# Performance work log

Hardware: AMD Instinct MI355X
Metric: run time of the kernel (lower is better)

## Reference

```python
import jax, jax.numpy as jnp
import numpy as np

# ---- geometry constants (from init_kwargs options) ----
VIEWS, NDET, NX, NY = 360, 736, 512, 512
DVOX, DDET = 0.7, 1.2858
DSO, DOD = 595.0, 490.6
DSD = DSO + DOD
STEP = 0.0174533
END_ANGLE = STEP * VIEWS  # ~2*pi
EXTENT = 1


def _compute_indices():
    """CPU port of PixelIndexCal_cuda (fanflat mode, extent=1).
    Returns flat int64 indices of shape [NX*NY*VIEWS] (pixel-major, view inner)."""
    sVx, sVy = DVOX * NX, DVOX * NY
    alphas = np.linspace(0.0, END_ANGLE, VIEWS, endpoint=False)
    indX, indY = np.meshgrid(np.arange(NX, dtype=np.float64),
                             np.arange(NY, dtype=np.float64), indexing='ij')
    idx_all = np.empty((NX * NY, VIEWS), dtype=np.int64)
    for a in range(VIEWS):
        alpha = -alphas[a]
        c, s = np.cos(alpha), np.sin(alpha)
        P0x = -(sVx / 2 - DVOX / 2)
        P0y = sVy / 2 - DVOX / 2
        rot = lambda px, py: (px * c + py * s, -px * s + py * c)
        Px_, Py_ = rot(P0x, P0y)
        Pxx, Pxy = rot(P0x + DVOX, P0y)
        Pyx, Pyy = rot(P0x, P0y - DVOX)
        Py_, Pxy, Pyy = Py_ / DDET, Pxy / DDET, Pyy / DDET
        dXx, dXy = Pxx - Px_, Pxy - Py_
        dYx, dYy = Pyx - Px_, Pyy - Py_
        # per-pixel rotated coords
        Pix = Px_ + indX * dXx + indY * dYx
        Piy = Py_ + indX * dXy + indY * dYy
        # fanflat: source at (DSO, 0); ray hits detector plane at x = DSO-DSD
        vectX = Pix - DSO
        t = -DSD / vectX
        det = Piy * t + NDET / 2.0
        det = np.clip(det, 1.0, NDET - 2.0)
        idx_all[:, a] = (det + NDET * a).astype(np.int64).ravel()
    return idx_all.reshape(-1)


def _conv(x, w, b):
    y = jax.lax.conv_general_dilated(x, w, (1, 1), 'SAME',
                                     dimension_numbers=('NCHW', 'OIHW', 'NCHW'))
    return y + b[None, :, None, None]


def setup_inputs() -> dict:
    key = jax.random.key(0)
    ks = jax.random.split(key, 16)
    lin_std = 1.0 / np.sqrt(NDET)
    conv_std = 1.0 / np.sqrt(64 * 9)
    inp = {
        'x': jax.random.normal(ks[0], (1, 1, VIEWS, NDET), jnp.float32),
        'indices': jnp.asarray(_compute_indices()),
        'w1': jax.random.normal(ks[1], (NDET, NDET), jnp.float32) * lin_std,
        'b1': jnp.zeros((NDET,), jnp.float32),
        'w2': jax.random.normal(ks[2], (NDET, NDET), jnp.float32) * lin_std,
        'b2': jnp.zeros((NDET,), jnp.float32),
        'conv_in_w': jax.random.normal(ks[3], (64, 1, 3, 3), jnp.float32) * (1.0 / 3.0),
        'conv_in_b': jnp.zeros((64,), jnp.float32),
        'blk_w1': jax.random.normal(ks[4], (11, 64, 64, 3, 3), jnp.float32) * conv_std,
        'blk_b1': jnp.zeros((11, 64), jnp.float32),
        'blk_w2': jax.random.normal(ks[5], (11, 64, 64, 3, 3), jnp.float32) * conv_std,
        'blk_b2': jnp.zeros((11, 64), jnp.float32),
        'conv_out_w': jax.random.normal(ks[6], (1, 64, 3, 3), jnp.float32) * conv_std,
        'conv_out_b': jnp.zeros((1,), jnp.float32),
    }
    return inp


def reference(x, indices, w1, b1, w2, b2, conv_in_w, conv_in_b,
              blk_w1, blk_b1, blk_w2, blk_b2, conv_out_w, conv_out_b):
    # convf: two per-detector-row Linear+ReLU over last dim (nDetecU)
    h = jax.nn.relu(x @ w1.T + b1)
    h = jax.nn.relu(h @ w2.T + b2)
    # BackProjNet (learn=False): gather + sum over views, scale, flip
    sino = h.reshape(-1, 1, VIEWS * NDET)
    g = sino[:, :, indices]                         # [B,1,NX*NY*VIEWS]
    g = g.reshape(-1, 1, NX * NY, VIEWS * EXTENT)
    img = g.sum(axis=3) * ((END_ANGLE - 0.0) / (2 * VIEWS * EXTENT))
    img = img.reshape(-1, 1, NX, NY)
    img = jnp.flip(img, axis=(2, 3))
    # rCNN refinement: conv(1->64)+ReLU, 11 residual blocks, conv(64->1)
    y = jax.nn.relu(_conv(img, conv_in_w, conv_in_b))
    for i in range(11):
        z = _conv(y, blk_w1[i], blk_b1[i])
        z = jax.nn.relu(z)
        z = _conv(z, blk_w2[i], blk_b2[i])
        y = jax.nn.relu(y + z)
    out = _conv(y, conv_out_w, conv_out_b)
    return out
```

## Files before the change

kernel.cpp:

```cpp
#include <hip/hip_runtime.h>

#define VIEWS 360
#define NDET 736
#define NX 512
#define NY 512
#define NPIX (NX * NY)

typedef unsigned short u16;
typedef __attribute__((ext_vector_type(8))) short bf16x8;
typedef __attribute__((ext_vector_type(4))) float f32x4;

__device__ __forceinline__ u16 f2bf(float f) {
  unsigned u = __float_as_uint(f);
  return (u16)((u + 0x7fffu + ((u >> 16) & 1u)) >> 16);
}

__global__ __launch_bounds__(256) void linear_relu_kernel(
    const float* __restrict__ in, const float* __restrict__ w,
    const float* __restrict__ b, float* __restrict__ out) {
  __shared__ __align__(16) float xin[NDET];
  const int v = blockIdx.x;
  const float4* src4 = (const float4*)(in + v * NDET);
  float4* dst4 = (float4*)xin;
  for (int k = threadIdx.x; k < NDET / 4; k += 256) dst4[k] = src4[k];
  __syncthreads();

  for (int d = threadIdx.x; d < NDET; d += 256) {
    const float4* w4 = (const float4*)(w + d * NDET);
    float acc = 0.f;
#pragma unroll 8
    for (int k = 0; k < NDET / 4; ++k) {
      float4 xv = ((const float4*)xin)[k];
      float4 wv = w4[k];
      acc = fmaf(xv.x, wv.x, acc);
      acc = fmaf(xv.y, wv.y, acc);
      acc = fmaf(xv.z, wv.z, acc);
      acc = fmaf(xv.w, wv.w, acc);
    }
    out[v * NDET + d] = fmaxf(acc + b[d], 0.f);
  }
}

__global__ __launch_bounds__(256) void backproj_kernel(
    const float* __restrict__ sino, const int* __restrict__ idx,
    float* __restrict__ img) {
  __shared__ int lidx[256 * 77];
  const int t = threadIdx.x;
  const int p_base = blockIdx.x * 256;

  float a0 = 0.f, a1 = 0.f, a2 = 0.f, a3 = 0.f;

#pragma unroll 1
  for (int c = 0; c < 5; ++c) {
    if (c) __syncthreads();
#pragma unroll
    for (int k = 0; k < 18; ++k) {
      const int f = k * 256 + t;
      const int row = f / 18, col4 = f % 18;
      int4 v = *(const int4*)&idx[(size_t)(p_base + row) * VIEWS + c * 72 +
                                  col4 * 4];
      int* dst = &lidx[row * 77 + col4 * 4];
      dst[0] = v.x; dst[1] = v.y; dst[2] = v.z; dst[3] = v.w;
    }
    __syncthreads();
    const int* myrow = &lidx[t * 77];
#pragma unroll
    for (int j = 0; j < 72; j += 4) {
      a0 += sino[myrow[j + 0]];
      a1 += sino[myrow[j + 1]];
      a2 += sino[myrow[j + 2]];
      a3 += sino[myrow[j + 3]];
    }
  }

  const int p = p_base + t;
  const int ix = p >> 9, iy = p & 511;
  img[(NX - 1 - ix) * NY + (NY - 1 - iy)] =
      ((a0 + a1) + (a2 + a3)) * 0.00872665f;
}

__device__ __forceinline__ void load9(const float* __restrict__ base, int gx,
                                      int gy, float v[9]) {
  const bool xm = gx > 0, xp = gx < NX - 1, ym = gy > 0, yp = gy < NY - 1;
  const float* c = base + gy * NX + gx;
  v[0] = (ym && xm) ? c[-NX - 1] : 0.f;
  v[1] = (ym)       ? c[-NX]     : 0.f;
  v[2] = (ym && xp) ? c[-NX + 1] : 0.f;
  v[3] = (xm)       ? c[-1]      : 0.f;
  v[4] =               c[0];
  v[5] = (xp)       ? c[1]       : 0.f;
  v[6] = (yp && xm) ? c[NX - 1]  : 0.f;
  v[7] = (yp)       ? c[NX]      : 0.f;
  v[8] = (yp && xp) ? c[NX + 1]  : 0.f;
}

__device__ __forceinline__ float dot9(float a, const float v[9],
                                      const float* __restrict__ w) {
  a = fmaf(v[0], w[0], a);
  a = fmaf(v[1], w[1], a);
  a = fmaf(v[2], w[2], a);
  a = fmaf(v[3], w[3], a);
  a = fmaf(v[4], w[4], a);
  a = fmaf(v[5], w[5], a);
  a = fmaf(v[6], w[6], a);
  a = fmaf(v[7], w[7], a);
  a = fmaf(v[8], w[8], a);
  return a;
}

__global__ __launch_bounds__(256) void conv_in_kernel(
    const float* __restrict__ in, const float* __restrict__ w,
    const float* __restrict__ b, float* __restrict__ out) {
  const int p = blockIdx.x * 256 + threadIdx.x;
  const int gx = p & (NX - 1), gy = p >> 9;
  float v[9];
  load9(in, gx, gy, v);
  float4* o = (float4*)(out + (size_t)p * 64);
#pragma unroll
  for (int oq = 0; oq < 16; ++oq) {
    float4 r;
    r.x = fmaxf(dot9(b[oq * 4 + 0], v, w + (oq * 4 + 0) * 9), 0.f);
    r.y = fmaxf(dot9(b[oq * 4 + 1], v, w + (oq * 4 + 1) * 9), 0.f);
    r.z = fmaxf(dot9(b[oq * 4 + 2], v, w + (oq * 4 + 2) * 9), 0.f);
    r.w = fmaxf(dot9(b[oq * 4 + 3], v, w + (oq * 4 + 3) * 9), 0.f);
    o[oq] = r;
  }
}

__global__ __launch_bounds__(256) void prep_weights_kernel(
    const float* __restrict__ bw1, const float* __restrict__ bw2,
    u16* __restrict__ wR) {
  const int g = blockIdx.x * 256 + threadIdx.x;
  if (g >= 22 * 36864) return;
  const int li = g / 36864, r1 = g % 36864;
  const int s = r1 / 2048, r2 = r1 % 2048;
  const int lane = r2 / 32, r3 = r2 % 32;
  const int mf = r3 / 8, j = r3 % 8;
  const int kb = s / 9, tap = s % 9;
  const int kg = lane >> 4, n = lane & 15;
  const int oc = mf * 16 + n;
  const int ic = kb * 32 + kg * 8 + j;
  const float* src = (li < 11) ? bw1 + li * 36864 : bw2 + (li - 11) * 36864;
  wR[g] = f2bf(src[(oc * 64 + ic) * 9 + tap]);
}

template <int IN_BF, int OUT_BF, int RELU, int ADDRES>
__global__ __launch_bounds__(256, 4) void conv64_mfma(
    const void* __restrict__ in_, const u16* __restrict__ wA,
    const float* __restrict__ bias, const float* __restrict__ res,
    void* __restrict__ out_) {
  __shared__ __align__(16) u16 lds[6 * 66 * 32];
  const int xb = (blockIdx.x & 7) * 64;
  const int yb = (int)(blockIdx.x >> 3) * 4;
  const int tid = threadIdx.x;
  const int wv = tid >> 6;
  const int lane = tid & 63;
  const int n = lane & 15;
  const int kg = lane >> 4;

  f32x4 acc[4][4];
#pragma unroll
  for (int i = 0; i < 4; ++i)
#pragma unroll
    for (int j = 0; j < 4; ++j) acc[i][j] = (f32x4){0.f, 0.f, 0.f, 0.f};

#pragma unroll 1
  for (int kb = 0; kb < 2; ++kb) {
    if (kb) __syncthreads();
#pragma unroll
    for (int it = 0; it < 7; ++it) {
      const int g = it * 256 + tid;
      if (g < 1584) {
        const int icq = g & 3;
        const int xr = g >> 2;
        const int x66 = xr % 66;
        const int r = xr / 66;
        const int y = yb - 1 + r;
        const int x = xb - 1 + x66;
        uint4 d = {0u, 0u, 0u, 0u};
        if ((unsigned)y < 512u && (unsigned)x < 512u) {
          const size_t gi =
              ((size_t)((y << 9) + x)) * 64 + kb * 32 + icq * 8;
          if (IN_BF) {
            d = *(const uint4*)&((const u16*)in_)[gi];
          } else {
            const float* s = &((const float*)in_)[gi];
            float4 f0 = *(const float4*)s;
            float4 f1 = *(const float4*)(s + 4);
            d.x = (unsigned)f2bf(f0.x) | ((unsigned)f2bf(f0.y) << 16);
            d.y = (unsigned)f2bf(f0.z) | ((unsigned)f2bf(f0.w) << 16);
            d.z = (unsigned)f2bf(f1.x) | ((unsigned)f2bf(f1.y) << 16);
            d.w = (unsigned)f2bf(f1.z) | ((unsigned)f2bf(f1.w) << 16);
          }
        }
        const int slot = icq ^ ((x66 >> 1) & 3);
        *(uint4*)&lds[(xr * 4 + slot) * 8] = d;
      }
    }
    __syncthreads();

#pragma unroll 3
    for (int tap = 0; tap < 9; ++tap) {
      const int s = kb * 9 + tap;
      bf16x8 av[4];
#pragma unroll
      for (int mf = 0; mf < 4; ++mf)
        av[mf] = *(const bf16x8*)&wA[((size_t)s * 64 + lane) * 32 + mf * 8];

      const int r = wv + tap / 3;
      const int dxp1 = tap % 3;

      bf16x8 bfr[4];
#pragma unroll
      for (int nf = 0; nf < 4; ++nf) {
        const int xi = dxp1 + nf * 16 + n;
        const int slot = kg ^ ((xi >> 1) & 3);
        bfr[nf] = *(const bf16x8*)&lds[((r * 66 + xi) * 4 + slot) * 8];
      }
#pragma unroll
      for (int mf = 0; mf < 4; ++mf)
#pragma unroll
        for (int nf = 0; nf < 4; ++nf)
          acc[mf][nf] = __builtin_amdgcn_mfma_f32_16x16x32_bf16(
              av[mf], bfr[nf], acc[mf][nf], 0, 0, 0);
    }
  }

  const int y = yb + wv;
#pragma unroll
  for (int mf = 0; mf < 4; ++mf) {
    const float4 bv = *(const float4*)&bias[mf * 16 + kg * 4];
#pragma unroll
    for (int nf = 0; nf < 4; ++nf) {
      const int x = xb + nf * 16 + n;
      const size_t base = ((size_t)((y << 9) + x)) * 64 + mf * 16 + kg * 4;
      float v0 = acc[mf][nf][0] + bv.x;
      float v1 = acc[mf][nf][1] + bv.y;
      float v2 = acc[mf][nf][2] + bv.z;
      float v3 = acc[mf][nf][3] + bv.w;
      if (ADDRES) {
        float4 rr = *(const float4*)&res[base];
        v0 += rr.x; v1 += rr.y; v2 += rr.z; v3 += rr.w;
      }
      if (RELU) {
        v0 = fmaxf(v0, 0.f); v1 = fmaxf(v1, 0.f);
        v2 = fmaxf(v2, 0.f); v3 = fmaxf(v3, 0.f);
      }
      if (OUT_BF) {
        uint2 pk;
        pk.x = (unsigned)f2bf(v0) | ((unsigned)f2bf(v1) << 16);
        pk.y = (unsigned)f2bf(v2) | ((unsigned)f2bf(v3) << 16);
        *(uint2*)&((u16*)out_)[base] = pk;
      } else {
        *(float4*)&((float*)out_)[base] = (float4){v0, v1, v2, v3};
      }
    }
  }
}

__global__ __launch_bounds__(256) void conv_out_kernel(
    const float* __restrict__ in, const float* __restrict__ w,
    const float* __restrict__ b, float* __restrict__ out) {
  const int p = blockIdx.x * 256 + threadIdx.x;
  const int gx = p & (NX - 1), gy = p >> 9;
  float a = b[0];
#pragma unroll
  for (int ty = 0; ty < 3; ++ty) {
#pragma unroll
    for (int tx = 0; tx < 3; ++tx) {
      const int yy = gy + ty - 1, xx = gx + tx - 1;
      if ((unsigned)yy < 512u && (unsigned)xx < 512u) {
        const float4* q = (const float4*)(in + ((size_t)((yy << 9) + xx)) * 64);
        const int tap = ty * 3 + tx;
#pragma unroll
        for (int i = 0; i < 16; ++i) {
          float4 d = q[i];
          a = fmaf(d.x, w[(i * 4 + 0) * 9 + tap], a);
          a = fmaf(d.y, w[(i * 4 + 1) * 9 + tap], a);
          a = fmaf(d.z, w[(i * 4 + 2) * 9 + tap], a);
          a = fmaf(d.w, w[(i * 4 + 3) * 9 + tap], a);
        }
      }
    }
  }
  out[p] = a;
}

extern "C" void kernel_launch(void* const* d_in, const int* in_sizes, int n_in,
                              void* d_out, int out_size, void* d_ws,
                              size_t ws_size, hipStream_t stream) {
  const float* x      = (const float*)d_in[0];
  const int*   indices= (const int*)d_in[1];
  const float* w1     = (const float*)d_in[2];
  const float* b1     = (const float*)d_in[3];
  const float* w2     = (const float*)d_in[4];
  const float* b2     = (const float*)d_in[5];
  const float* cin_w  = (const float*)d_in[6];
  const float* cin_b  = (const float*)d_in[7];
  const float* bw1    = (const float*)d_in[8];
  const float* bb1    = (const float*)d_in[9];
  const float* bw2    = (const float*)d_in[10];
  const float* bb2    = (const float*)d_in[11];
  const float* cout_w = (const float*)d_in[12];
  const float* cout_b = (const float*)d_in[13];

  float* ws   = (float*)d_ws;
  float* h1   = ws;
  float* h2   = h1 + VIEWS * NDET;
  float* img  = h2 + VIEWS * NDET;
  float* yf   = img + NPIX;
  u16*  zb    = (u16*)(yf + 64 * NPIX);
  u16*  wAll  = zb + 64 * NPIX;

  prep_weights_kernel<<<(22 * 36864 + 255) / 256, 256, 0, stream>>>(bw1, bw2,
                                                                    wAll);
  linear_relu_kernel<<<VIEWS, 256, 0, stream>>>(x, w1, b1, h1);
  linear_relu_kernel<<<VIEWS, 256, 0, stream>>>(h1, w2, b2, h2);
  backproj_kernel<<<NPIX / 256, 256, 0, stream>>>(h2, indices, img);
  conv_in_kernel<<<NPIX / 256, 256, 0, stream>>>(img, cin_w, cin_b, yf);

  for (int i = 0; i < 11; ++i) {
    conv64_mfma<0, 1, 1, 0><<<1024, 256, 0, stream>>>(
        yf, wAll + i * 36864, bb1 + i * 64, nullptr, zb);
    conv64_mfma<1, 0, 1, 1><<<1024, 256, 0, stream>>>(
        zb, wAll + (11 + i) * 36864, bb2 + i * 64, yf, yf);
  }
  conv_out_kernel<<<NPIX / 256, 256, 0, stream>>>(yf, cout_w, cout_b,
                                                  (float*)d_out);
}
```

Measured before the change: 1.835 ms.

## Keep bf16 activation copy, use direct global-to-LDS loads, batch linear rows

The residual stream is now also stored as bf16, so the first conv of each block reads a bf16 input instead of converting fp32 on the fly. The conv tile load uses global_load_lds with a zero-padding buffer for out-of-bounds pixels, which removes the register staging and the branchy zero fill. The linear layers now process four views per block so each weight row is reused across four rows of input. This adds an extra bf16 write per block and more workspace, and it relies on the direct-to-LDS write order matching the swizzled layout.

```diff
diff --git a/kernel.cpp b/kernel.cpp
--- a/kernel.cpp
+++ b/kernel.cpp
@@ -14,30 +14,71 @@
   unsigned u = __float_as_uint(f);
   return (u16)((u + 0x7fffu + ((u >> 16) & 1u)) >> 16);
 }
-
-__global__ __launch_bounds__(256) void linear_relu_kernel(
+__device__ __forceinline__ float bf2f(u16 v) {
+  return __uint_as_float(((unsigned)v) << 16);
+}
+
+__device__ __forceinline__ void gload_lds16(const void* g, void* l) {
+  __builtin_amdgcn_global_load_lds(
+      (const __attribute__((address_space(1))) void*)g,
+      (__attribute__((address_space(3))) void*)l, 16, 0, 0);
+}
+
+__global__ __launch_bounds__(256) void linear_relu4_kernel(
     const float* __restrict__ in, const float* __restrict__ w,
     const float* __restrict__ b, float* __restrict__ out) {
-  __shared__ __align__(16) float xin[NDET];
-  const int v = blockIdx.x;
-  const float4* src4 = (const float4*)(in + v * NDET);
-  float4* dst4 = (float4*)xin;
-  for (int k = threadIdx.x; k < NDET / 4; k += 256) dst4[k] = src4[k];
+  __shared__ __align__(16) float xin[4][NDET];
+  const int v0 = blockIdx.x * 4;
+  const int t = threadIdx.x;
+  for (int k = t; k < 4 * (NDET / 4); k += 256) {
+    const int row = k / (NDET / 4), c4 = k % (NDET / 4);
+    ((float4*)xin[row])[c4] = ((const float4*)(in + (size_t)(v0 + row) * NDET))[c4];
+  }
   __syncthreads();
 
-  for (int d = threadIdx.x; d < NDET; d += 256) {
-    const float4* w4 = (const float4*)(w + d * NDET);
-    float acc = 0.f;
-#pragma unroll 8
-    for (int k = 0; k < NDET / 4; ++k) {
-      float4 xv = ((const float4*)xin)[k];
-      float4 wv = w4[k];
-      acc = fmaf(xv.x, wv.x, acc);
-      acc = fmaf(xv.y, wv.y, acc);
-      acc = fmaf(xv.z, wv.z, acc);
-      acc = fmaf(xv.w, wv.w, acc);
-    }
-    out[v * NDET + d] = fmaxf(acc + b[d], 0.f);
+  const bool has2 = (t < NDET - 512);
+  const float4* w0 = (const float4*)(w + (size_t)t * NDET);
+  const float4* w1 = (const float4*)(w + (size_t)(t + 256) * NDET);
+  const float4* w2 = (const float4*)(w + (size_t)(has2 ? t + 512 : t) * NDET);
+
+  float acc[3][4];
+#pragma unroll
+  for (int j = 0; j < 3; ++j)
+#pragma unroll
+    for (int v = 0; v < 4; ++v) acc[j][v] = 0.f;
+
+#pragma unroll 2
+  for (int k = 0; k < NDET / 4; ++k) {
+    float4 xv0 = ((const float4*)xin[0])[k];
+    float4 xv1 = ((const float4*)xin[1])[k];
+    float4 xv2 = ((const float4*)xin[2])[k];
+    float4 xv3 = ((const float4*)xin[3])[k];
+    float4 wv;
+    wv = w0[k];
+    acc[0][0] = fmaf(xv0.x, wv.x, fmaf(xv0.y, wv.y, fmaf(xv0.z, wv.z, fmaf(xv0.w, wv.w, acc[0][0]))));
+    acc[0][1] = fmaf(xv1.x, wv.x, fmaf(xv1.y, wv.y, fmaf(xv1.z, wv.z, fmaf(xv1.w, wv.w, acc[0][1]))));
+    acc[0][2] = fmaf(xv2.x, wv.x, fmaf(xv2.y, wv.y, fmaf(xv2.z, wv.z, fmaf(xv2.w, wv.w, acc[0][2]))));
+    acc[0][3] = fmaf(xv3.x, wv.x, fmaf(xv3.y, wv.y, fmaf(xv3.z, wv.z, fmaf(xv3.w, wv.w, acc[0][3]))));
+    wv = w1[k];
+    acc[1][0] = fmaf(xv0.x, wv.x, fmaf(xv0.y, wv.y, fmaf(xv0.z, wv.z, fmaf(xv0.w, wv.w, acc[1][0]))));
+    acc[1][1] = fmaf(xv1.x, wv.x, fmaf(xv1.y, wv.y, fmaf(xv1.z, wv.z, fmaf(xv1.w, wv.w, acc[1][1]))));
+    acc[1][2] = fmaf(xv2.x, wv.x, fmaf(xv2.y, wv.y, fmaf(xv2.z, wv.z, fmaf(xv2.w, wv.w, acc[1][2]))));
+    acc[1][3] = fmaf(xv3.x, wv.x, fmaf(xv3.y, wv.y, fmaf(xv3.z, wv.z, fmaf(xv3.w, wv.w, acc[1][3]))));
+    wv = w2[k];
+    acc[2][0] = fmaf(xv0.x, wv.x, fmaf(xv0.y, wv.y, fmaf(xv0.z, wv.z, fmaf(xv0.w, wv.w, acc[2][0]))));
+    acc[2][1] = fmaf(xv1.x, wv.x, fmaf(xv1.y, wv.y, fmaf(xv1.z, wv.z, fmaf(xv1.w, wv.w, acc[2][1]))));
+    acc[2][2] = fmaf(xv2.x, wv.x, fmaf(xv2.y, wv.y, fmaf(xv2.z, wv.z, fmaf(xv2.w, wv.w, acc[2][2]))));
+    acc[2][3] = fmaf(xv3.x, wv.x, fmaf(xv3.y, wv.y, fmaf(xv3.z, wv.z, fmaf(xv3.w, wv.w, acc[2][3]))));
+  }
+
+  const float b0 = b[t], b1 = b[t + 256];
+  const float b2v = has2 ? b[t + 512] : 0.f;
+#pragma unroll
+  for (int v = 0; v < 4; ++v) {
+    float* o = out + (size_t)(v0 + v) * NDET;
+    o[t] = fmaxf(acc[0][v] + b0, 0.f);
+    o[t + 256] = fmaxf(acc[1][v] + b1, 0.f);
+    if (has2) o[t + 512] = fmaxf(acc[2][v] + b2v, 0.f);
   }
 }
 
@@ -110,20 +151,28 @@
 
 __global__ __launch_bounds__(256) void conv_in_kernel(
     const float* __restrict__ in, const float* __restrict__ w,
-    const float* __restrict__ b, float* __restrict__ out) {
+    const float* __restrict__ b, float* __restrict__ outf,
+    u16* __restrict__ outb) {
   const int p = blockIdx.x * 256 + threadIdx.x;
   const int gx = p & (NX - 1), gy = p >> 9;
   float v[9];
   load9(in, gx, gy, v);
-  float4* o = (float4*)(out + (size_t)p * 64);
-#pragma unroll
-  for (int oq = 0; oq < 16; ++oq) {
-    float4 r;
-    r.x = fmaxf(dot9(b[oq * 4 + 0], v, w + (oq * 4 + 0) * 9), 0.f);
-    r.y = fmaxf(dot9(b[oq * 4 + 1], v, w + (oq * 4 + 1) * 9), 0.f);
-    r.z = fmaxf(dot9(b[oq * 4 + 2], v, w + (oq * 4 + 2) * 9), 0.f);
-    r.w = fmaxf(dot9(b[oq * 4 + 3], v, w + (oq * 4 + 3) * 9), 0.f);
-    o[oq] = r;
+  float4* of = (float4*)(outf + (size_t)p * 64);
+  uint4* ob = (uint4*)(outb + (size_t)p * 64);
+#pragma unroll
+  for (int oq = 0; oq < 8; ++oq) {
+    float f[8];
+#pragma unroll
+    for (int c = 0; c < 8; ++c)
+      f[c] = fmaxf(dot9(b[oq * 8 + c], v, w + (oq * 8 + c) * 9), 0.f);
+    of[oq * 2 + 0] = (float4){f[0], f[1], f[2], f[3]};
+    of[oq * 2 + 1] = (float4){f[4], f[5], f[6], f[7]};
+    uint4 pk;
+    pk.x = (unsigned)f2bf(f[0]) | ((unsigned)f2bf(f[1]) << 16);
+    pk.y = (unsigned)f2bf(f[2]) | ((unsigned)f2bf(f[3]) << 16);
+    pk.z = (unsigned)f2bf(f[4]) | ((unsigned)f2bf(f[5]) << 16);
+    pk.w = (unsigned)f2bf(f[6]) | ((unsigned)f2bf(f[7]) << 16);
+    ob[oq] = pk;
   }
 }
 
@@ -132,6 +181,7 @@
     u16* __restrict__ wR) {
   const int g = blockIdx.x * 256 + threadIdx.x;
   if (g >= 22 * 36864) return;
+  if (g < 32) wR[22 * 36864 + g] = 0;
   const int li = g / 36864, r1 = g % 36864;
   const int s = r1 / 2048, r2 = r1 % 2048;
   const int lane = r2 / 32, r3 = r2 % 32;
@@ -144,11 +194,12 @@
   wR[g] = f2bf(src[(oc * 64 + ic) * 9 + tap]);
 }
 
-template <int IN_BF, int OUT_BF, int RELU, int ADDRES>
+template <int ADDRES, int DUALOUT>
 __global__ __launch_bounds__(256, 4) void conv64_mfma(
-    const void* __restrict__ in_, const u16* __restrict__ wA,
+    const u16* __restrict__ in_, const u16* __restrict__ wA,
     const float* __restrict__ bias, const float* __restrict__ res,
-    void* __restrict__ out_) {
+    u16* __restrict__ outb, float* __restrict__ outf,
+    const u16* __restrict__ zpad) {
   __shared__ __align__(16) u16 lds[6 * 66 * 32];
   const int xb = (blockIdx.x & 7) * 64;
   const int yb = (int)(blockIdx.x >> 3) * 4;
@@ -170,31 +221,18 @@
 #pragma unroll
     for (int it = 0; it < 7; ++it) {
       const int g = it * 256 + tid;
-      if (g < 1584) {
-        const int icq = g & 3;
+      if (it < 6 || g < 1584) {
+        const int j = g & 3;
         const int xr = g >> 2;
         const int x66 = xr % 66;
         const int r = xr / 66;
         const int y = yb - 1 + r;
         const int x = xb - 1 + x66;
-        uint4 d = {0u, 0u, 0u, 0u};
-        if ((unsigned)y < 512u && (unsigned)x < 512u) {
-          const size_t gi =
-              ((size_t)((y << 9) + x)) * 64 + kb * 32 + icq * 8;
-          if (IN_BF) {
-            d = *(const uint4*)&((const u16*)in_)[gi];
-          } else {
-            const float* s = &((const float*)in_)[gi];
-            float4 f0 = *(const float4*)s;
-            float4 f1 = *(const float4*)(s + 4);
-            d.x = (unsigned)f2bf(f0.x) | ((unsigned)f2bf(f0.y) << 16);
-            d.y = (unsigned)f2bf(f0.z) | ((unsigned)f2bf(f0.w) << 16);
-            d.z = (unsigned)f2bf(f1.x) | ((unsigned)f2bf(f1.y) << 16);
-            d.w = (unsigned)f2bf(f1.z) | ((unsigned)f2bf(f1.w) << 16);
-          }
-        }
-        const int slot = icq ^ ((x66 >> 1) & 3);
-        *(uint4*)&lds[(xr * 4 + slot) * 8] = d;
+        const int icq = j ^ ((x66 >> 1) & 3);
+        const u16* src = zpad;
+        if ((unsigned)y < 512u && (unsigned)x < 512u)
+          src = in_ + ((size_t)((y << 9) + x)) * 64 + kb * 32 + icq * 8;
+        gload_lds16(src, &lds[(size_t)(g & ~63) * 8]);
       }
     }
     __syncthreads();
@@ -242,17 +280,14 @@
         float4 rr = *(const float4*)&res[base];
         v0 += rr.x; v1 += rr.y; v2 += rr.z; v3 += rr.w;
       }
-      if (RELU) {
-        v0 = fmaxf(v0, 0.f); v1 = fmaxf(v1, 0.f);
-        v2 = fmaxf(v2, 0.f); v3 = fmaxf(v3, 0.f);
-      }
-      if (OUT_BF) {
-        uint2 pk;
-        pk.x = (unsigned)f2bf(v0) | ((unsigned)f2bf(v1) << 16);
-        pk.y = (unsigned)f2bf(v2) | ((unsigned)f2bf(v3) << 16);
-        *(uint2*)&((u16*)out_)[base] = pk;
-      } else {
-        *(float4*)&((float*)out_)[base] = (float4){v0, v1, v2, v3};
+      v0 = fmaxf(v0, 0.f); v1 = fmaxf(v1, 0.f);
+      v2 = fmaxf(v2, 0.f); v3 = fmaxf(v3, 0.f);
+      uint2 pk;
+      pk.x = (unsigned)f2bf(v0) | ((unsigned)f2bf(v1) << 16);
+      pk.y = (unsigned)f2bf(v2) | ((unsigned)f2bf(v3) << 16);
+      *(uint2*)&outb[base] = pk;
+      if (DUALOUT) {
+        *(float4*)&outf[base] = (float4){v0, v1, v2, v3};
       }
     }
   }
@@ -309,21 +344,23 @@
   float* h2   = h1 + VIEWS * NDET;
   float* img  = h2 + VIEWS * NDET;
   float* yf   = img + NPIX;
-  u16*  zb    = (u16*)(yf + 64 * NPIX);
-  u16*  wAll  = zb + 64 * NPIX;
+  u16*  ybf   = (u16*)(yf + (size_t)64 * NPIX);
+  u16*  zb    = ybf + (size_t)64 * NPIX;
+  u16*  wAll  = zb + (size_t)64 * NPIX;
+  u16*  zpad  = wAll + 22 * 36864;
 
   prep_weights_kernel<<<(22 * 36864 + 255) / 256, 256, 0, stream>>>(bw1, bw2,
                                                                     wAll);
-  linear_relu_kernel<<<VIEWS, 256, 0, stream>>>(x, w1, b1, h1);
-  linear_relu_kernel<<<VIEWS, 256, 0, stream>>>(h1, w2, b2, h2);
+  linear_relu4_kernel<<<VIEWS / 4, 256, 0, stream>>>(x, w1, b1, h1);
+  linear_relu4_kernel<<<VIEWS / 4, 256, 0, stream>>>(h1, w2, b2, h2);
   backproj_kernel<<<NPIX / 256, 256, 0, stream>>>(h2, indices, img);
-  conv_in_kernel<<<NPIX / 256, 256, 0, stream>>>(img, cin_w, cin_b, yf);
+  conv_in_kernel<<<NPIX / 256, 256, 0, stream>>>(img, cin_w, cin_b, yf, ybf);
 
   for (int i = 0; i < 11; ++i) {
-    conv64_mfma<0, 1, 1, 0><<<1024, 256, 0, stream>>>(
-        yf, wAll + i * 36864, bb1 + i * 64, nullptr, zb);
-    conv64_mfma<1, 0, 1, 1><<<1024, 256, 0, stream>>>(
-        zb, wAll + (11 + i) * 36864, bb2 + i * 64, yf, yf);
+    conv64_mfma<0, 0><<<1024, 256, 0, stream>>>(
+        ybf, wAll + i * 36864, bb1 + i * 64, nullptr, zb, nullptr, zpad);
+    conv64_mfma<1, 1><<<1024, 256, 0, stream>>>(
+        zb, wAll + (11 + i) * 36864, bb2 + i * 64, yf, ybf, yf, zpad);
   }
   conv_out_kernel<<<NPIX / 256, 256, 0, stream>>>(yf, cout_w, cout_b,
                                                   (float*)d_out);
```

Result: slower. 1.927 ms (+5.0%).

## Process four views per block in linear layers and coalesce conv weight loads

Applied to the files above, without the earlier changes.

The linear+ReLU kernel now handles four sinogram rows per block, reusing each weight row load across four input vectors, and each thread computes up to three output detectors. This cuts the number of blocks and the redundant reads of the weight matrix. The conv weight layout is also reordered so per-mf fragments are contiguous across lanes, which gives coalesced 16-byte loads. The linear kernel's grid drops to 90 blocks, so occupancy on a large GPU is low.

```diff
diff --git a/kernel.cpp b/kernel.cpp
--- a/kernel.cpp
+++ b/kernel.cpp
@@ -15,29 +15,61 @@
   return (u16)((u + 0x7fffu + ((u >> 16) & 1u)) >> 16);
 }
 
-__global__ __launch_bounds__(256) void linear_relu_kernel(
+__global__ __launch_bounds__(256) void linear_relu4_kernel(
     const float* __restrict__ in, const float* __restrict__ w,
     const float* __restrict__ b, float* __restrict__ out) {
-  __shared__ __align__(16) float xin[NDET];
-  const int v = blockIdx.x;
-  const float4* src4 = (const float4*)(in + v * NDET);
-  float4* dst4 = (float4*)xin;
-  for (int k = threadIdx.x; k < NDET / 4; k += 256) dst4[k] = src4[k];
+  __shared__ __align__(16) float xin[4][NDET];
+  const int v0 = blockIdx.x * 4;
+  const int t = threadIdx.x;
+  for (int k = t; k < 4 * (NDET / 4); k += 256) {
+    const int row = k / (NDET / 4), c4 = k % (NDET / 4);
+    ((float4*)xin[row])[c4] = ((const float4*)(in + (size_t)(v0 + row) * NDET))[c4];
+  }
   __syncthreads();
 
-  for (int d = threadIdx.x; d < NDET; d += 256) {
-    const float4* w4 = (const float4*)(w + d * NDET);
-    float acc = 0.f;
-#pragma unroll 8
-    for (int k = 0; k < NDET / 4; ++k) {
-      float4 xv = ((const float4*)xin)[k];
-      float4 wv = w4[k];
-      acc = fmaf(xv.x, wv.x, acc);
-      acc = fmaf(xv.y, wv.y, acc);
-      acc = fmaf(xv.z, wv.z, acc);
-      acc = fmaf(xv.w, wv.w, acc);
-    }
-    out[v * NDET + d] = fmaxf(acc + b[d], 0.f);
+  const bool has2 = (t < NDET - 512);
+  const float4* w0 = (const float4*)(w + (size_t)t * NDET);
+  const float4* w1 = (const float4*)(w + (size_t)(t + 256) * NDET);
+  const float4* w2 = (const float4*)(w + (size_t)(has2 ? t + 512 : t) * NDET);
+
+  float acc[3][4];
+#pragma unroll
+  for (int j = 0; j < 3; ++j)
+#pragma unroll
+    for (int v = 0; v < 4; ++v) acc[j][v] = 0.f;
+
+#pragma unroll 2
+  for (int k = 0; k < NDET / 4; ++k) {
+    float4 xv0 = ((const float4*)xin[0])[k];
+    float4 xv1 = ((const float4*)xin[1])[k];
+    float4 xv2 = ((const float4*)xin[2])[k];
+    float4 xv3 = ((const float4*)xin[3])[k];
+    float4 wv;
+    wv = w0[k];
+    acc[0][0] = fmaf(xv0.x, wv.x, fmaf(xv0.y, wv.y, fmaf(xv0.z, wv.z, fmaf(xv0.w, wv.w, acc[0][0]))));
+    acc[0][1] = fmaf(xv1.x, wv.x, fmaf(xv1.y, wv.y, fmaf(xv1.z, wv.z, fmaf(xv1.w, wv.w, acc[0][1]))));
+    acc[0][2] = fmaf(xv2.x, wv.x, fmaf(xv2.y, wv.y, fmaf(xv2.z, wv.z, fmaf(xv2.w, wv.w, acc[0][2]))));
+    acc[0][3] = fmaf(xv3.x, wv.x, fmaf(xv3.y, wv.y, fmaf(xv3.z, wv.z, fmaf(xv3.w, wv.w, acc[0][3]))));
+    wv = w1[k];
+    acc[1][0] = fmaf(xv0.x, wv.x, fmaf(xv0.y, wv.y, fmaf(xv0.z, wv.z, fmaf(xv0.w, wv.w, acc[1][0]))));
+    acc[1][1] = fmaf(xv1.x, wv.x, fmaf(xv1.y, wv.y, fmaf(xv1.z, wv.z, fmaf(xv1.w, wv.w, acc[1][1]))));
+    acc[1][2] = fmaf(xv2.x, wv.x, fmaf(xv2.y, wv.y, fmaf(xv2.z, wv.z, fmaf(xv2.w, wv.w, acc[1][2]))));
+    acc[1][3] = fmaf(xv3.x, wv.x, fmaf(xv3.y, wv.y, fmaf(xv3.z, wv.z, fmaf(xv3.w, wv.w, acc[1][3]))));
+    wv = w2[k];
+    acc[2][0] = fmaf(xv0.x, wv.x, fmaf(xv0.y, wv.y, fmaf(xv0.z, wv.z, fmaf(xv0.w, wv.w, acc[2][0]))));
+    acc[2][1] = fmaf(xv1.x, wv.x, fmaf(xv1.y, wv.y, fmaf(xv1.z, wv.z, fmaf(xv1.w, wv.w, acc[2][1]))));
+    acc[2][2] = fmaf(xv2.x, wv.x, fmaf(xv2.y, wv.y, fmaf(xv2.z, wv.z, fmaf(xv2.w, wv.w, acc[2][2]))));
+    acc[2][3] = fmaf(xv3.x, wv.x, fmaf(xv3.y, wv.y, fmaf(xv3.z, wv.z, fmaf(xv3.w, wv.w, acc[2][3]))));
+  }
+
+  const float b0 = b[t], b1 = b[t + 256];
+  const float b2v = has2 ? b[t + 512] : 0.f;
+#pragma unroll
+  for (int v = 0; v < 4; ++v) {
+    float* o = out + (size_t)(v0 + v) * NDET;
+    o[t] = fmaxf(acc[0][v] + b0, 0.f);
+    o[t + 256] = fmaxf(acc[1][v] + b1, 0.f);
+    if (has2) o[t + 512] = fmaxf(acc[2][v] + b2v, 0.f);
   }
 }
 
@@ -134,8 +166,8 @@
   if (g >= 22 * 36864) return;
   const int li = g / 36864, r1 = g % 36864;
   const int s = r1 / 2048, r2 = r1 % 2048;
-  const int lane = r2 / 32, r3 = r2 % 32;
-  const int mf = r3 / 8, j = r3 % 8;
+  const int mf = r2 / 512, r3 = r2 % 512;
+  const int lane = r3 / 8, j = r3 % 8;
   const int kb = s / 9, tap = s % 9;
   const int kg = lane >> 4, n = lane & 15;
   const int oc = mf * 16 + n;
@@ -205,7 +237,7 @@
       bf16x8 av[4];
 #pragma unroll
       for (int mf = 0; mf < 4; ++mf)
-        av[mf] = *(const bf16x8*)&wA[((size_t)s * 64 + lane) * 32 + mf * 8];
+        av[mf] = *(const bf16x8*)&wA[(size_t)s * 2048 + mf * 512 + lane * 8];
 
       const int r = wv + tap / 3;
       const int dxp1 = tap % 3;
@@ -309,13 +341,13 @@
   float* h2   = h1 + VIEWS * NDET;
   float* img  = h2 + VIEWS * NDET;
   float* yf   = img + NPIX;
-  u16*  zb    = (u16*)(yf + 64 * NPIX);
-  u16*  wAll  = zb + 64 * NPIX;
+  u16*  zb    = (u16*)(yf + (size_t)64 * NPIX);
+  u16*  wAll  = zb + (size_t)64 * NPIX;
 
   prep_weights_kernel<<<(22 * 36864 + 255) / 256, 256, 0, stream>>>(bw1, bw2,
                                                                     wAll);
-  linear_relu_kernel<<<VIEWS, 256, 0, stream>>>(x, w1, b1, h1);
-  linear_relu_kernel<<<VIEWS, 256, 0, stream>>>(h1, w2, b2, h2);
+  linear_relu4_kernel<<<VIEWS / 4, 256, 0, stream>>>(x, w1, b1, h1);
+  linear_relu4_kernel<<<VIEWS / 4, 256, 0, stream>>>(h1, w2, b2, h2);
   backproj_kernel<<<NPIX / 256, 256, 0, stream>>>(h2, indices, img);
   conv_in_kernel<<<NPIX / 256, 256, 0, stream>>>(img, cin_w, cin_b, yf);
 
```

Result: slower. 1.896 ms (+3.4%).

## Load bf16 conv input directly to LDS and double-buffer both channel halves

Applied to the files above, without the earlier changes.

The second conv of each residual block now issues global_load_lds DMA loads straight into shared memory, bypassing registers. It issues both 32-channel halves up front into two LDS buffers and waits on partial vmcnt so compute on the first half overlaps the second half's load. Out-of-bounds pixels read from a small zeroed pad buffer, and the swizzle is applied on the source side. This doubles LDS use per block and lowers the occupancy target to 3 blocks per SM, and it relies on hand-written waitcnt and barrier assembly.

```diff
diff --git a/kernel.cpp b/kernel.cpp
--- a/kernel.cpp
+++ b/kernel.cpp
@@ -13,6 +13,12 @@
 __device__ __forceinline__ u16 f2bf(float f) {
   unsigned u = __float_as_uint(f);
   return (u16)((u + 0x7fffu + ((u >> 16) & 1u)) >> 16);
+}
+
+__device__ __forceinline__ void gload_lds16(const void* g, void* l) {
+  __builtin_amdgcn_global_load_lds(
+      (const __attribute__((address_space(1))) void*)g,
+      (__attribute__((address_space(3))) void*)l, 16, 0, 0);
 }
 
 __global__ __launch_bounds__(256) void linear_relu_kernel(
@@ -132,6 +138,7 @@
     u16* __restrict__ wR) {
   const int g = blockIdx.x * 256 + threadIdx.x;
   if (g >= 22 * 36864) return;
+  if (g < 32) wR[22 * 36864 + g] = 0;
   const int li = g / 36864, r1 = g % 36864;
   const int s = r1 / 2048, r2 = r1 % 2048;
   const int lane = r2 / 32, r3 = r2 % 32;
@@ -144,11 +151,42 @@
   wR[g] = f2bf(src[(oc * 64 + ic) * 9 + tap]);
 }
 
-template <int IN_BF, int OUT_BF, int RELU, int ADDRES>
-__global__ __launch_bounds__(256, 4) void conv64_mfma(
-    const void* __restrict__ in_, const u16* __restrict__ wA,
-    const float* __restrict__ bias, const float* __restrict__ res,
-    void* __restrict__ out_) {
+__device__ __forceinline__ void compute_half(const u16* lds,
+                                             const u16* __restrict__ wA,
+                                             int kb, int wv, int lane,
+                                             f32x4 acc[4][4]) {
+  const int n = lane & 15;
+  const int kg = lane >> 4;
+#pragma unroll 3
+  for (int tap = 0; tap < 9; ++tap) {
+    const int s = kb * 9 + tap;
+    bf16x8 av[4];
+#pragma unroll
+    for (int mf = 0; mf < 4; ++mf)
+      av[mf] = *(const bf16x8*)&wA[((size_t)s * 64 + lane) * 32 + mf * 8];
+
+    const int r = wv + tap / 3;
+    const int dxp1 = tap % 3;
+
+    bf16x8 bfr[4];
+#pragma unroll
+    for (int nf = 0; nf < 4; ++nf) {
+      const int xi = dxp1 + nf * 16 + n;
+      const int slot = kg ^ ((xi >> 1) & 3);
+      bfr[nf] = *(const bf16x8*)&lds[((r * 66 + xi) * 4 + slot) * 8];
+    }
+#pragma unroll
+    for (int mf = 0; mf < 4; ++mf)
+#pragma unroll
+      for (int nf = 0; nf < 4; ++nf)
+        acc[mf][nf] = __builtin_amdgcn_mfma_f32_16x16x32_bf16(
+            av[mf], bfr[nf], acc[mf][nf], 0, 0, 0);
+  }
+}
+
+__global__ __launch_bounds__(256, 4) void conv64_c1(
+    const float* __restrict__ in_, const u16* __restrict__ wA,
+    const float* __restrict__ bias, u16* __restrict__ out_) {
   __shared__ __align__(16) u16 lds[6 * 66 * 32];
   const int xb = (blockIdx.x & 7) * 64;
   const int yb = (int)(blockIdx.x >> 3) * 4;
@@ -179,51 +217,21 @@
         const int x = xb - 1 + x66;
         uint4 d = {0u, 0u, 0u, 0u};
         if ((unsigned)y < 512u && (unsigned)x < 512u) {
-          const size_t gi =
-              ((size_t)((y << 9) + x)) * 64 + kb * 32 + icq * 8;
-          if (IN_BF) {
-            d = *(const uint4*)&((const u16*)in_)[gi];
-          } else {
-            const float* s = &((const float*)in_)[gi];
-            float4 f0 = *(const float4*)s;
-            float4 f1 = *(const float4*)(s + 4);
-            d.x = (unsigned)f2bf(f0.x) | ((unsigned)f2bf(f0.y) << 16);
-            d.y = (unsigned)f2bf(f0.z) | ((unsigned)f2bf(f0.w) << 16);
-            d.z = (unsigned)f2bf(f1.x) | ((unsigned)f2bf(f1.y) << 16);
-            d.w = (unsigned)f2bf(f1.z) | ((unsigned)f2bf(f1.w) << 16);
-          }
+          const size_t gi = ((size_t)((y << 9) + x)) * 64 + kb * 32 + icq * 8;
+          const float* s = &in_[gi];
+          float4 f0 = *(const float4*)s;
+          float4 f1 = *(const float4*)(s + 4);
+          d.x = (unsigned)f2bf(f0.x) | ((unsigned)f2bf(f0.y) << 16);
+          d.y = (unsigned)f2bf(f0.z) | ((unsigned)f2bf(f0.w) << 16);
+          d.z = (unsigned)f2bf(f1.x) | ((unsigned)f2bf(f1.y) << 16);
+          d.w = (unsigned)f2bf(f1.z) | ((unsigned)f2bf(f1.w) << 16);
         }
         const int slot = icq ^ ((x66 >> 1) & 3);
         *(uint4*)&lds[(xr * 4 + slot) * 8] = d;
       }
     }
     __syncthreads();
-
-#pragma unroll 3
-    for (int tap = 0; tap < 9; ++tap) {
-      const int s = kb * 9 + tap;
-      bf16x8 av[4];
-#pragma unroll
-      for (int mf = 0; mf < 4; ++mf)
-        av[mf] = *(const bf16x8*)&wA[((size_t)s * 64 + lane) * 32 + mf * 8];
-
-      const int r = wv + tap / 3;
-      const int dxp1 = tap % 3;
-
-      bf16x8 bfr[4];
-#pragma unroll
-      for (int nf = 0; nf < 4; ++nf) {
-        const int xi = dxp1 + nf * 16 + n;
-        const int slot = kg ^ ((xi >> 1) & 3);
-        bfr[nf] = *(const bf16x8*)&lds[((r * 66 + xi) * 4 + slot) * 8];
-      }
-#pragma unroll
-      for (int mf = 0; mf < 4; ++mf)
-#pragma unroll
-        for (int nf = 0; nf < 4; ++nf)
-          acc[mf][nf] = __builtin_amdgcn_mfma_f32_16x16x32_bf16(
-              av[mf], bfr[nf], acc[mf][nf], 0, 0, 0);
-    }
+    compute_half(lds, wA, kb, wv, lane, acc);
   }
 
   const int y = yb + wv;
@@ -234,26 +242,80 @@
     for (int nf = 0; nf < 4; ++nf) {
       const int x = xb + nf * 16 + n;
       const size_t base = ((size_t)((y << 9) + x)) * 64 + mf * 16 + kg * 4;
-      float v0 = acc[mf][nf][0] + bv.x;
-      float v1 = acc[mf][nf][1] + bv.y;
-      float v2 = acc[mf][nf][2] + bv.z;
-      float v3 = acc[mf][nf][3] + bv.w;
-      if (ADDRES) {
-        float4 rr = *(const float4*)&res[base];
-        v0 += rr.x; v1 += rr.y; v2 += rr.z; v3 += rr.w;
+      float v0 = fmaxf(acc[mf][nf][0] + bv.x, 0.f);
+      float v1 = fmaxf(acc[mf][nf][1] + bv.y, 0.f);
+      float v2 = fmaxf(acc[mf][nf][2] + bv.z, 0.f);
+      float v3 = fmaxf(acc[mf][nf][3] + bv.w, 0.f);
+      uint2 pk;
+      pk.x = (unsigned)f2bf(v0) | ((unsigned)f2bf(v1) << 16);
+      pk.y = (unsigned)f2bf(v2) | ((unsigned)f2bf(v3) << 16);
+      *(uint2*)&out_[base] = pk;
+    }
+  }
+}
+
+__global__ __launch_bounds__(256, 3) void conv64_pipe(
+    const u16* __restrict__ in_, const u16* __restrict__ wA,
+    const float* __restrict__ bias, const float* __restrict__ res,
+    float* __restrict__ out_, const u16* __restrict__ zpad) {
+  __shared__ __align__(16) u16 lds[2][6 * 66 * 32];
+  const int xb = (blockIdx.x & 7) * 64;
+  const int yb = (int)(blockIdx.x >> 3) * 4;
+  const int tid = threadIdx.x;
+  const int wv = tid >> 6;
+  const int lane = tid & 63;
+  const int n = lane & 15;
+  const int kg = lane >> 4;
+
+#pragma unroll
+  for (int kb = 0; kb < 2; ++kb) {
+#pragma unroll
+    for (int it = 0; it < 7; ++it) {
+      const int g = it * 256 + tid;
+      if (g < 1584) {
+        const int j = g & 3;
+        const int xr = g >> 2;
+        const int x66 = xr % 66;
+        const int r = xr / 66;
+        const int y = yb - 1 + r;
+        const int x = xb - 1 + x66;
+        const int icq = j ^ ((x66 >> 1) & 3);
+        const u16* src = zpad;
+        if ((unsigned)y < 512u && (unsigned)x < 512u)
+          src = in_ + ((size_t)((y << 9) + x)) * 64 + kb * 32 + icq * 8;
+        gload_lds16(src, &lds[kb][(size_t)(g & ~63) * 8]);
       }
-      if (RELU) {
-        v0 = fmaxf(v0, 0.f); v1 = fmaxf(v1, 0.f);
-        v2 = fmaxf(v2, 0.f); v3 = fmaxf(v3, 0.f);
-      }
-      if (OUT_BF) {
-        uint2 pk;
-        pk.x = (unsigned)f2bf(v0) | ((unsigned)f2bf(v1) << 16);
-        pk.y = (unsigned)f2bf(v2) | ((unsigned)f2bf(v3) << 16);
-        *(uint2*)&((u16*)out_)[base] = pk;
-      } else {
-        *(float4*)&((float*)out_)[base] = (float4){v0, v1, v2, v3};
-      }
+    }
+  }
+
+  f32x4 acc[4][4];
+#pragma unroll
+  for (int i = 0; i < 4; ++i)
+#pragma unroll
+    for (int j = 0; j < 4; ++j) acc[i][j] = (f32x4){0.f, 0.f, 0.f, 0.f};
+
+  asm volatile("s_waitcnt vmcnt(6)\n\ts_barrier" ::: "memory");
+  __builtin_amdgcn_sched_barrier(0);
+  compute_half(lds[0], wA, 0, wv, lane, acc);
+
+  asm volatile("s_waitcnt vmcnt(0)\n\ts_barrier" ::: "memory");
+  __builtin_amdgcn_sched_barrier(0);
+  compute_half(lds[1], wA, 1, wv, lane, acc);
+
+  const int y = yb + wv;
+#pragma unroll
+  for (int mf = 0; mf < 4; ++mf) {
+    const float4 bv = *(const float4*)&bias[mf * 16 + kg * 4];
+#pragma unroll
+    for (int nf = 0; nf < 4; ++nf) {
+      const int x = xb + nf * 16 + n;
+      const size_t base = ((size_t)((y << 9) + x)) * 64 + mf * 16 + kg * 4;
+      float4 rr = *(const float4*)&res[base];
+      float v0 = fmaxf(acc[mf][nf][0] + bv.x + rr.x, 0.f);
+      float v1 = fmaxf(acc[mf][nf][1] + bv.y + rr.y, 0.f);
+      float v2 = fmaxf(acc[mf][nf][2] + bv.z + rr.z, 0.f);
+      float v3 = fmaxf(acc[mf][nf][3] + bv.w + rr.w, 0.f);
+      *(float4*)&out_[base] = (float4){v0, v1, v2, v3};
     }
   }
 }
@@ -309,8 +371,9 @@
   float* h2   = h1 + VIEWS * NDET;
   float* img  = h2 + VIEWS * NDET;
   float* yf   = img + NPIX;
-  u16*  zb    = (u16*)(yf + 64 * NPIX);
-  u16*  wAll  = zb + 64 * NPIX;
+  u16*  zb    = (u16*)(yf + (size_t)64 * NPIX);
+  u16*  wAll  = zb + (size_t)64 * NPIX;
+  u16*  zpad  = wAll + 22 * 36864;
 
   prep_weights_kernel<<<(22 * 36864 + 255) / 256, 256, 0, stream>>>(bw1, bw2,
                                                                     wAll);
@@ -320,10 +383,10 @@
   conv_in_kernel<<<NPIX / 256, 256, 0, stream>>>(img, cin_w, cin_b, yf);
 
   for (int i = 0; i < 11; ++i) {
-    conv64_mfma<0, 1, 1, 0><<<1024, 256, 0, stream>>>(
-        yf, wAll + i * 36864, bb1 + i * 64, nullptr, zb);
-    conv64_mfma<1, 0, 1, 1><<<1024, 256, 0, stream>>>(
-        zb, wAll + (11 + i) * 36864, bb2 + i * 64, yf, yf);
+    conv64_c1<<<1024, 256, 0, stream>>>(yf, wAll + i * 36864, bb1 + i * 64,
+                                        zb);
+    conv64_pipe<<<1024, 256, 0, stream>>>(zb, wAll + (11 + i) * 36864,
+                                          bb2 + i * 64, yf, yf, zpad);
   }
   conv_out_kernel<<<NPIX / 256, 256, 0, stream>>>(yf, cout_w, cout_b,
                                                   (float*)d_out);
```

Measured after the change: 1.871 ms. About the same (+2.0%).
